# Performance work log

Measured on AMD Instinct MI355X. Metric: run time of the kernel, lower is better.

The kernel has to match this reference:

```python
import jax, jax.numpy as jnp
import numpy as np

B, S, D_MODEL = 1, 4096, 1024
D_QK = 1024
H = 32
HEAD_D = D_QK // H      # 32
V_D = D_MODEL // H      # 32
K_CONV = 4
C_CONV = D_MODEL + 2 * D_QK  # 3072 (conv_type='full')


def setup_inputs() -> dict:
    key = jax.random.key(0)
    ks = jax.random.split(key, 7)
    s_in = 1.0 / np.sqrt(D_MODEL)
    return {
        "x": jax.random.normal(ks[0], (B, S, D_MODEL), jnp.float32),
        "Wqkv_w": jax.random.normal(ks[1], (2 * D_QK + D_MODEL, D_MODEL), jnp.float32) * s_in,
        "Wqkv_b": jax.random.normal(ks[2], (2 * D_QK + D_MODEL,), jnp.float32) * 0.01,
        "conv_w": jax.random.normal(ks[3], (C_CONV, 1, K_CONV), jnp.float32) * (1.0 / np.sqrt(K_CONV)),
        "conv_b": jax.random.normal(ks[4], (C_CONV,), jnp.float32) * 0.01,
        "out_w": jax.random.normal(ks[5], (D_MODEL, D_MODEL), jnp.float32) * s_in,
        "out_b": jax.random.normal(ks[6], (D_MODEL,), jnp.float32) * 0.01,
    }


def reference(x, Wqkv_w, Wqkv_b, conv_w, conv_b, out_w, out_b):
    # QKV projection: (B,S,3072)
    qkv = x @ Wqkv_w.T + Wqkv_b
    # depthwise causal conv over seq dim (torch pads k-1 both sides, truncates to S == left-pad k-1)
    z = qkv.transpose(0, 2, 1)  # (B,C,S)
    z = jax.lax.conv_general_dilated(
        z, conv_w, window_strides=(1,), padding=[(K_CONV - 1, 0)],
        dimension_numbers=("NCH", "OIH", "NCH"), feature_group_count=C_CONV)
    z = z + conv_b[None, :, None]
    qkv = jax.nn.silu(z).transpose(0, 2, 1)  # (B,S,C)

    qk = qkv[..., : 2 * D_QK].reshape(B, S, 2, H, HEAD_D)
    v = qkv[..., 2 * D_QK :].reshape(B, S, H, V_D)
    q, k = qk[:, :, 0], qk[:, :, 1]
    q = jax.nn.elu(q) + 1.0
    k = jax.nn.elu(k) + 1.0

    # linear attention via cumulative KV state: (B,S,H,D,Dv)
    kv = jnp.einsum("bshd,bsht->bshdt", k, v)
    kv = jnp.cumsum(kv, axis=1)
    k_cum = jnp.cumsum(k, axis=1)
    denom = jnp.einsum("bshd,bshd->bsh", q, k_cum)
    ctx = jnp.einsum("bshd,bshdt->bsht", q, kv) / denom[..., None]  # (B,S,H,Dv)

    out = ctx.reshape(B, S, D_MODEL) @ out_w.T + out_b
    return out
```

## Files before the change

### kernel.cpp

```cpp
#include <hip/hip_runtime.h>
#include <hip/hip_bf16.h>
#include <math.h>

#define S_LEN 4096
#define D_MODEL 1024
#define C_CONV 3072
#define H_HEADS 32
#define HEAD_D 32
#define V_D 32
#define K_CONV 4
#define CHUNK 64
#define NCH (S_LEN / CHUNK)
#define SC_STRIDE (HEAD_D * V_D + HEAD_D)

typedef __attribute__((ext_vector_type(8))) short short8;
typedef __attribute__((ext_vector_type(4))) float f32x4;

#define F4C(v, k) ((k) == 0 ? (v).x : (k) == 1 ? (v).y : (k) == 2 ? (v).z : (v).w)

__device__ __forceinline__ ushort f32_to_bf16_rne(float f) {
  unsigned u = __float_as_uint(f);
  unsigned rounding = 0x7FFFu + ((u >> 16) & 1u);
  return (ushort)((u + rounding) >> 16);
}

__device__ __forceinline__ void gload_lds16(const void* g, void* l) {
  __builtin_amdgcn_global_load_lds(
      (const __attribute__((address_space(1))) void*)g,
      (__attribute__((address_space(3))) void*)l, 16, 0, 0);
}

__global__ __launch_bounds__(256) void split_bf16(
    const float* __restrict__ in, ushort* __restrict__ hi,
    ushort* __restrict__ lo, int n4) {
  int i = blockIdx.x * 256 + threadIdx.x;
  const int stride = gridDim.x * 256;
  for (; i < n4; i += stride) {
    const float4 v = reinterpret_cast<const float4*>(in)[i];
    float arr[4] = {v.x, v.y, v.z, v.w};
    ushort hh[4], ll[4];
#pragma unroll
    for (int j = 0; j < 4; ++j) {
      const ushort hb = f32_to_bf16_rne(arr[j]);
      const float hf = __uint_as_float((unsigned)hb << 16);
      hh[j] = hb;
      ll[j] = f32_to_bf16_rne(arr[j] - hf);
    }
    ushort4 h = {hh[0], hh[1], hh[2], hh[3]};
    ushort4 lw = {ll[0], ll[1], ll[2], ll[3]};
    reinterpret_cast<ushort4*>(hi)[i] = h;
    reinterpret_cast<ushort4*>(lo)[i] = lw;
  }
}

#define GBM 128
#define GBK 32

template <int NF>
__global__ __launch_bounds__(256, 4) void gemm_nt_split3(
    const ushort* __restrict__ Ah, const ushort* __restrict__ Al,
    const ushort* __restrict__ Bh, const ushort* __restrict__ Bl,
    const float* __restrict__ bias, float* __restrict__ C,
    int M, int N, int K) {
  constexpr int BN = NF * 32;
  __shared__ ushort lds[8192 + 2 * BN * 32];
  ushort* sAh = lds;
  ushort* sAl = lds + 4096;
  ushort* sBh = lds + 8192;
  ushort* sBl = lds + 8192 + BN * 32;

  const int t = threadIdx.x;
  const int l = t & 63;
  const int w = t >> 6;
  const int wr = w >> 1;
  const int wc = w & 1;
  const int bm = blockIdx.y * GBM;
  const int bn = blockIdx.x * BN;
  const int r16 = l & 15;
  const int g = l >> 4;

  f32x4 acc[4][NF];
#pragma unroll
  for (int m = 0; m < 4; ++m)
#pragma unroll
    for (int n = 0; n < NF; ++n) acc[m][n] = {0.f, 0.f, 0.f, 0.f};

  auto stage = [&](const ushort* __restrict__ G, ushort* Lt, int base_row,
                   int k0, int nu ) {
    for (int u0 = 0; u0 < nu; u0 += 256) {
      const int u = u0 + t;
      const int row = u >> 2;
      const int sp = u & 3;
      const int sg = sp ^ ((row >> 1) & 3);
      gload_lds16(&G[(size_t)(base_row + row) * K + k0 + sg * 8], &Lt[u * 8]);
    }
  };

  for (int k0 = 0; k0 < K; k0 += GBK) {
    stage(Ah, sAh, bm, k0, 512);
    stage(Al, sAl, bm, k0, 512);
    stage(Bh, sBh, bn, k0, BN * 4);
    stage(Bl, sBl, bn, k0, BN * 4);
    __syncthreads();

    short8 afh[4], afl[4], bfh[NF], bfl[NF];
#pragma unroll
    for (int m = 0; m < 4; ++m) {
      const int arow = wr * 64 + m * 16 + r16;
      const int off = arow * 64 + (((g ^ ((arow >> 1) & 3))) << 4);
      afh[m] = *reinterpret_cast<const short8*>((const char*)sAh + off);
      afl[m] = *reinterpret_cast<const short8*>((const char*)sAl + off);
    }
#pragma unroll
    for (int n = 0; n < NF; ++n) {
      const int brow = wc * (NF * 16) + n * 16 + r16;
      const int off = brow * 64 + (((g ^ ((brow >> 1) & 3))) << 4);
      bfh[n] = *reinterpret_cast<const short8*>((const char*)sBh + off);
      bfl[n] = *reinterpret_cast<const short8*>((const char*)sBl + off);
    }
#pragma unroll
    for (int m = 0; m < 4; ++m)
#pragma unroll
      for (int n = 0; n < NF; ++n) {
        acc[m][n] = __builtin_amdgcn_mfma_f32_16x16x32_bf16(
            afh[m], bfh[n], acc[m][n], 0, 0, 0);
        acc[m][n] = __builtin_amdgcn_mfma_f32_16x16x32_bf16(
            afh[m], bfl[n], acc[m][n], 0, 0, 0);
        acc[m][n] = __builtin_amdgcn_mfma_f32_16x16x32_bf16(
            afl[m], bfh[n], acc[m][n], 0, 0, 0);
      }
    __syncthreads();
  }

#pragma unroll
  for (int n = 0; n < NF; ++n) {
    const int col = bn + wc * (NF * 16) + n * 16 + r16;
    const float bb = bias[col];
#pragma unroll
    for (int m = 0; m < 4; ++m) {
      const int row0 = bm + wr * 64 + m * 16 + g * 4;
#pragma unroll
      for (int j = 0; j < 4; ++j)
        C[(size_t)(row0 + j) * N + col] = acc[m][n][j] + bb;
    }
  }
}

__global__ __launch_bounds__(256) void conv_silu_act(
    const float* __restrict__ qkv, const float* __restrict__ conv_w,
    const float* __restrict__ conv_b, float* __restrict__ act) {
  const int gid = blockIdx.x * 256 + threadIdx.x;
  const int nc4 = C_CONV / 4;
  if (gid >= S_LEN * nc4) return;
  const int s = gid / nc4;
  const int c = (gid % nc4) * 4;

  float w[4][4];
#pragma unroll
  for (int cc = 0; cc < 4; ++cc) {
    const float4 wv = *reinterpret_cast<const float4*>(&conv_w[(c + cc) * 4]);
    w[cc][0] = wv.x; w[cc][1] = wv.y; w[cc][2] = wv.z; w[cc][3] = wv.w;
  }
  const float4 bv = *reinterpret_cast<const float4*>(&conv_b[c]);
  float z[4] = {bv.x, bv.y, bv.z, bv.w};

#pragma unroll
  for (int j = 0; j < 4; ++j) {
    const int sp = s - 3 + j;
    if (sp >= 0) {
      const float4 in = *reinterpret_cast<const float4*>(
          &qkv[(size_t)sp * C_CONV + c]);
      z[0] += in.x * w[0][j]; z[1] += in.y * w[1][j];
      z[2] += in.z * w[2][j]; z[3] += in.w * w[3][j];
    }
  }

  float out[4];
  const bool is_qk = (c < 2 * D_MODEL);
#pragma unroll
  for (int cc = 0; cc < 4; ++cc) {
    float a = z[cc] / (1.0f + expf(-z[cc]));
    if (is_qk) a = (a > 0.0f) ? (a + 1.0f) : expf(a);
    out[cc] = a;
  }
  float4 ov = {out[0], out[1], out[2], out[3]};
  *reinterpret_cast<float4*>(&act[(size_t)s * C_CONV + c]) = ov;
}

__global__ __launch_bounds__(256) void chunk_sums(
    const float* __restrict__ act, float* __restrict__ SC) {
  const int ch = blockIdx.x;
  const int h = blockIdx.y;
  const int t = threadIdx.x;
  __shared__ float ks[CHUNK][32];
  __shared__ float vs[CHUNK][36];

#pragma unroll
  for (int i = 0; i < 2; ++i) {
    int idx = t + 256 * i;
    int r = idx >> 3;
    int c0 = (idx & 7) * 4;
    const size_t row = (size_t)(ch * CHUNK + r) * C_CONV;
    const float4 kv4 = *reinterpret_cast<const float4*>(
        &act[row + D_MODEL + h * 32 + c0]);
    *reinterpret_cast<float4*>(&ks[r][c0]) = kv4;
    const float4 vv4 = *reinterpret_cast<const float4*>(
        &act[row + 2 * D_MODEL + h * 32 + c0]);
    *reinterpret_cast<float4*>(&vs[r][c0]) = vv4;
  }
  __syncthreads();

  const int d = t >> 3;
  const int c4 = (t & 7) * 4;
  float4 acc = {0.f, 0.f, 0.f, 0.f};
  float ksum = 0.f;
#pragma unroll 4
  for (int s = 0; s < CHUNK; ++s) {
    const float kv = ks[s][d];
    const float4 vv = *reinterpret_cast<const float4*>(&vs[s][c4]);
    acc.x += kv * vv.x; acc.y += kv * vv.y;
    acc.z += kv * vv.z; acc.w += kv * vv.w;
    ksum += kv;
  }
  float* out = &SC[(size_t)(ch * H_HEADS + h) * SC_STRIDE];
  *reinterpret_cast<float4*>(&out[d * 32 + c4]) = acc;
  if ((t & 7) == 0) out[1024 + d] = ksum;
}

__global__ __launch_bounds__(256) void chunk_prefix(
    const float* __restrict__ SC, float* __restrict__ SP) {
  const int h = blockIdx.x;
  const int t = threadIdx.x;
  for (int e = t; e < SC_STRIDE; e += 256) {
    float run = 0.f;
    for (int c = 0; c < NCH; ++c) {
      const size_t off = (size_t)(c * H_HEADS + h) * SC_STRIDE + e;
      SP[off] = run;
      run += SC[off];
    }
  }
}

__global__ __launch_bounds__(256) void chunk_ctx(
    const float* __restrict__ act, const float* __restrict__ SP,
    ushort* __restrict__ ctx_h, ushort* __restrict__ ctx_l) {
  const int ch = blockIdx.x;
  const int h = blockIdx.y;
  const int t = threadIdx.x;

  __shared__ float qs[CHUNK][36];
  __shared__ float ksT[32][68];
  __shared__ float vs[CHUNK][36];
  __shared__ float KVp[32][36];
  __shared__ float Amat[CHUNK][68];
  __shared__ float Kp[32];
  __shared__ float denomp[CHUNK][4];
  __shared__ float denom[CHUNK];

#pragma unroll
  for (int i = 0; i < 2; ++i) {
    const int idx = t + 256 * i;
    const int r = idx >> 3;
    const int c0 = (idx & 7) * 4;
    const size_t row = (size_t)(ch * CHUNK + r) * C_CONV;
    float4 v4;
    v4 = *reinterpret_cast<const float4*>(&act[row + h * 32 + c0]);
    *reinterpret_cast<float4*>(&qs[r][c0]) = v4;
    v4 = *reinterpret_cast<const float4*>(&act[row + D_MODEL + h * 32 + c0]);
    ksT[c0 + 0][r] = v4.x; ksT[c0 + 1][r] = v4.y;
    ksT[c0 + 2][r] = v4.z; ksT[c0 + 3][r] = v4.w;
    v4 = *reinterpret_cast<const float4*>(&act[row + 2 * D_MODEL + h * 32 + c0]);
    *reinterpret_cast<float4*>(&vs[r][c0]) = v4;
  }
  const float* sp = &SP[(size_t)(ch * H_HEADS + h) * SC_STRIDE];
  {
    const float4 v4 = *reinterpret_cast<const float4*>(&sp[t * 4]);
    *reinterpret_cast<float4*>(&KVp[t >> 3][(t & 7) * 4]) = v4;
  }
  if (t < 32) Kp[t] = sp[1024 + t];
  __syncthreads();

  {
    const int tm = t >> 4;
    const int tn = t & 15;
    float a1[4][4] = {{0.f}};
#pragma unroll
    for (int g = 0; g < 8; ++g) {
      const int d0 = g * 4;
      float4 qv[4], kq[4];
#pragma unroll
      for (int i = 0; i < 4; ++i)
        qv[i] = *reinterpret_cast<const float4*>(&qs[tm * 4 + i][d0]);
#pragma unroll
      for (int dd = 0; dd < 4; ++dd)
        kq[dd] = *reinterpret_cast<const float4*>(&ksT[d0 + dd][tn * 4]);
#pragma unroll
      for (int i = 0; i < 4; ++i)
#pragma unroll
        for (int dd = 0; dd < 4; ++dd) {
          const float qa = F4C(qv[i], dd);
          a1[i][0] += qa * kq[dd].x;
          a1[i][1] += qa * kq[dd].y;
          a1[i][2] += qa * kq[dd].z;
          a1[i][3] += qa * kq[dd].w;
        }
    }
#pragma unroll
    for (int i = 0; i < 4; ++i) {
      const int s = tm * 4 + i;
      float4 o;
      o.x = (tn * 4 + 0 <= s) ? a1[i][0] : 0.f;
      o.y = (tn * 4 + 1 <= s) ? a1[i][1] : 0.f;
      o.z = (tn * 4 + 2 <= s) ? a1[i][2] : 0.f;
      o.w = (tn * 4 + 3 <= s) ? a1[i][3] : 0.f;
      *reinterpret_cast<float4*>(&Amat[s][tn * 4]) = o;
    }
  }
  __syncthreads();

  {
    const int row = t & 63;
    const int qd = t >> 6;
    float part = 0.f;
#pragma unroll
    for (int j = 0; j < 16; ++j) part += Amat[row][qd * 16 + j];
    if (qd < 2) {
#pragma unroll
      for (int j = 0; j < 16; ++j)
        part += qs[row][qd * 16 + j] * Kp[qd * 16 + j];
    }
    denomp[row][qd] = part;
  }
  __syncthreads();
  if (t < CHUNK) {
    const float4 dp = *reinterpret_cast<const float4*>(&denomp[t][0]);
    denom[t] = dp.x + dp.y + dp.z + dp.w;
  }
  __syncthreads();

  {
    const int r2 = t >> 3;
    const int c4 = (t & 7) * 4;
    float a3[2][4] = {{0.f}};
#pragma unroll
    for (int sg = 0; sg < 16; ++sg) {
      const int s0 = sg * 4;
      float4 av[2];
      av[0] = *reinterpret_cast<const float4*>(&Amat[r2 * 2 + 0][s0]);
      av[1] = *reinterpret_cast<const float4*>(&Amat[r2 * 2 + 1][s0]);
      float4 vv[4];
#pragma unroll
      for (int ss = 0; ss < 4; ++ss)
        vv[ss] = *reinterpret_cast<const float4*>(&vs[s0 + ss][c4]);
#pragma unroll
      for (int i = 0; i < 2; ++i)
#pragma unroll
        for (int ss = 0; ss < 4; ++ss) {
          const float aa = F4C(av[i], ss);
          a3[i][0] += aa * vv[ss].x;
          a3[i][1] += aa * vv[ss].y;
          a3[i][2] += aa * vv[ss].z;
          a3[i][3] += aa * vv[ss].w;
        }
    }
#pragma unroll
    for (int g = 0; g < 8; ++g) {
      const int d0 = g * 4;
      float4 qv[2];
      qv[0] = *reinterpret_cast<const float4*>(&qs[r2 * 2 + 0][d0]);
      qv[1] = *reinterpret_cast<const float4*>(&qs[r2 * 2 + 1][d0]);
      float4 kv[4];
#pragma unroll
      for (int dd = 0; dd < 4; ++dd)
        kv[dd] = *reinterpret_cast<const float4*>(&KVp[d0 + dd][c4]);
#pragma unroll
      for (int i = 0; i < 2; ++i)
#pragma unroll
        for (int dd = 0; dd < 4; ++dd) {
          const float qa = F4C(qv[i], dd);
          a3[i][0] += qa * kv[dd].x;
          a3[i][1] += qa * kv[dd].y;
          a3[i][2] += qa * kv[dd].z;
          a3[i][3] += qa * kv[dd].w;
        }
    }
#pragma unroll
    for (int i = 0; i < 2; ++i) {
      const int srow = r2 * 2 + i;
      const float dn = denom[srow];
      const size_t off = (size_t)(ch * CHUNK + srow) * D_MODEL + h * 32 + c4;
      ushort4 hv, lv;
      ushort hh[4], ll[4];
#pragma unroll
      for (int c = 0; c < 4; ++c) {
        const float val = a3[i][c] / dn;
        const ushort hb = f32_to_bf16_rne(val);
        hh[c] = hb;
        ll[c] = f32_to_bf16_rne(val - __uint_as_float((unsigned)hb << 16));
      }
      hv.x = hh[0]; hv.y = hh[1]; hv.z = hh[2]; hv.w = hh[3];
      lv.x = ll[0]; lv.y = ll[1]; lv.z = ll[2]; lv.w = ll[3];
      *reinterpret_cast<ushort4*>(&ctx_h[off]) = hv;
      *reinterpret_cast<ushort4*>(&ctx_l[off]) = lv;
    }
  }
}

extern "C" void kernel_launch(void* const* d_in, const int* in_sizes, int n_in,
                              void* d_out, int out_size, void* d_ws, size_t ws_size,
                              hipStream_t stream) {
  const float* x      = (const float*)d_in[0];
  const float* Wqkv_w = (const float*)d_in[1];
  const float* Wqkv_b = (const float*)d_in[2];
  const float* conv_w = (const float*)d_in[3];
  const float* conv_b = (const float*)d_in[4];
  const float* out_w  = (const float*)d_in[5];
  const float* out_b  = (const float*)d_in[6];
  float* out = (float*)d_out;

  char* ws = (char*)d_ws;
  float*  qkv_raw = (float*)(ws);
  float*  SC      = (float*)(ws);
  float*  SP      = (float*)(ws + 8650752);
  ushort* ch      = (ushort*)(ws + 17301504);
  ushort* cl      = (ushort*)(ws + 25690112);
  float*  act     = (float*)(ws + 50331648);
  ushort* xh      = (ushort*)(ws + 50331648);
  ushort* xl      = (ushort*)(ws + 58720256);
  ushort* wh      = (ushort*)(ws + 67108864);
  ushort* wl      = (ushort*)(ws + 73400320);
  ushort* oh      = (ushort*)(ws + 50331648);
  ushort* ol      = (ushort*)(ws + 52428800);

  split_bf16<<<2048, 256, 0, stream>>>(x, xh, xl, S_LEN * D_MODEL / 4);
  split_bf16<<<2048, 256, 0, stream>>>(Wqkv_w, wh, wl, C_CONV * D_MODEL / 4);

  {
    dim3 grid(C_CONV / 128, S_LEN / GBM);
    gemm_nt_split3<4><<<grid, 256, 0, stream>>>(xh, xl, wh, wl, Wqkv_b,
                                                qkv_raw, S_LEN, C_CONV,
                                                D_MODEL);
  }
  {
    int total = S_LEN * (C_CONV / 4);
    conv_silu_act<<<(total + 255) / 256, 256, 0, stream>>>(qkv_raw, conv_w,
                                                           conv_b, act);
  }
  {
    dim3 grid(NCH, H_HEADS);
    chunk_sums<<<grid, 256, 0, stream>>>(act, SC);
  }
  chunk_prefix<<<H_HEADS, 256, 0, stream>>>(SC, SP);
  {
    dim3 grid(NCH, H_HEADS);
    chunk_ctx<<<grid, 256, 0, stream>>>(act, SP, ch, cl);
  }
  split_bf16<<<1024, 256, 0, stream>>>(out_w, oh, ol, D_MODEL * D_MODEL / 4);
  {
    dim3 grid(D_MODEL / 64, S_LEN / GBM);
    gemm_nt_split3<2><<<grid, 256, 0, stream>>>(ch, cl, oh, ol, out_b, out,
                                                S_LEN, D_MODEL, D_MODEL);
  }
}
```

Before: 325.9 us.

## Merge input splits, parallelize chunk prefix, widen output GEMM tile

Fuses the two bf16 hi/lo split launches for x and Wqkv into one kernel, saving a launch. Spreads chunk_prefix over a 2D grid so each thread handles one state element instead of looping over several per head, which raises parallelism in that serial scan. Also switches the output projection GEMM from a 64-wide to a 128-wide N tile. The wider tile halves the block count to 256, which may under-fill the GPU's compute units.

```diff
diff --git a/kernel.cpp b/kernel.cpp
--- a/kernel.cpp
+++ b/kernel.cpp
@@ -30,26 +30,43 @@
       (__attribute__((address_space(3))) void*)l, 16, 0, 0);
 }
 
+__device__ __forceinline__ void split_one4(const float* __restrict__ in,
+                                           ushort* __restrict__ hi,
+                                           ushort* __restrict__ lo, int i) {
+  const float4 v = reinterpret_cast<const float4*>(in)[i];
+  float arr[4] = {v.x, v.y, v.z, v.w};
+  ushort hh[4], ll[4];
+#pragma unroll
+  for (int j = 0; j < 4; ++j) {
+    const ushort hb = f32_to_bf16_rne(arr[j]);
+    const float hf = __uint_as_float((unsigned)hb << 16);
+    hh[j] = hb;
+    ll[j] = f32_to_bf16_rne(arr[j] - hf);
+  }
+  ushort4 h = {hh[0], hh[1], hh[2], hh[3]};
+  ushort4 lw = {ll[0], ll[1], ll[2], ll[3]};
+  reinterpret_cast<ushort4*>(hi)[i] = h;
+  reinterpret_cast<ushort4*>(lo)[i] = lw;
+}
+
 __global__ __launch_bounds__(256) void split_bf16(
     const float* __restrict__ in, ushort* __restrict__ hi,
     ushort* __restrict__ lo, int n4) {
   int i = blockIdx.x * 256 + threadIdx.x;
   const int stride = gridDim.x * 256;
-  for (; i < n4; i += stride) {
-    const float4 v = reinterpret_cast<const float4*>(in)[i];
-    float arr[4] = {v.x, v.y, v.z, v.w};
-    ushort hh[4], ll[4];
-#pragma unroll
-    for (int j = 0; j < 4; ++j) {
-      const ushort hb = f32_to_bf16_rne(arr[j]);
-      const float hf = __uint_as_float((unsigned)hb << 16);
-      hh[j] = hb;
-      ll[j] = f32_to_bf16_rne(arr[j] - hf);
-    }
-    ushort4 h = {hh[0], hh[1], hh[2], hh[3]};
-    ushort4 lw = {ll[0], ll[1], ll[2], ll[3]};
-    reinterpret_cast<ushort4*>(hi)[i] = h;
-    reinterpret_cast<ushort4*>(lo)[i] = lw;
+  for (; i < n4; i += stride) split_one4(in, hi, lo, i);
+}
+
+__global__ __launch_bounds__(256) void split_bf16_x2(
+    const float* __restrict__ a, ushort* __restrict__ ah,
+    ushort* __restrict__ al, int n4a,
+    const float* __restrict__ b, ushort* __restrict__ bh,
+    ushort* __restrict__ bl, int n4b) {
+  const int gid = blockIdx.x * 256 + threadIdx.x;
+  if (gid < n4a) {
+    split_one4(a, ah, al, gid);
+  } else if (gid < n4a + n4b) {
+    split_one4(b, bh, bl, gid - n4a);
   }
 }
 
@@ -229,15 +246,14 @@
 
 __global__ __launch_bounds__(256) void chunk_prefix(
     const float* __restrict__ SC, float* __restrict__ SP) {
-  const int h = blockIdx.x;
-  const int t = threadIdx.x;
-  for (int e = t; e < SC_STRIDE; e += 256) {
-    float run = 0.f;
-    for (int c = 0; c < NCH; ++c) {
-      const size_t off = (size_t)(c * H_HEADS + h) * SC_STRIDE + e;
-      SP[off] = run;
-      run += SC[off];
-    }
+  const int h = blockIdx.y;
+  const int e = blockIdx.x * 256 + threadIdx.x;
+  if (e >= SC_STRIDE) return;
+  float run = 0.f;
+  for (int c = 0; c < NCH; ++c) {
+    const size_t off = (size_t)(c * H_HEADS + h) * SC_STRIDE + e;
+    SP[off] = run;
+    run += SC[off];
   }
 }
 
@@ -432,8 +448,9 @@
   ushort* oh      = (ushort*)(ws + 50331648);
   ushort* ol      = (ushort*)(ws + 52428800);
 
-  split_bf16<<<2048, 256, 0, stream>>>(x, xh, xl, S_LEN * D_MODEL / 4);
-  split_bf16<<<2048, 256, 0, stream>>>(Wqkv_w, wh, wl, C_CONV * D_MODEL / 4);
+  split_bf16_x2<<<7168, 256, 0, stream>>>(
+      x, xh, xl, S_LEN * D_MODEL / 4,
+      Wqkv_w, wh, wl, C_CONV * D_MODEL / 4);
 
   {
     dim3 grid(C_CONV / 128, S_LEN / GBM);
@@ -450,15 +467,18 @@
     dim3 grid(NCH, H_HEADS);
     chunk_sums<<<grid, 256, 0, stream>>>(act, SC);
   }
-  chunk_prefix<<<H_HEADS, 256, 0, stream>>>(SC, SP);
+  {
+    dim3 grid((SC_STRIDE + 255) / 256, H_HEADS);
+    chunk_prefix<<<grid, 256, 0, stream>>>(SC, SP);
+  }
   {
     dim3 grid(NCH, H_HEADS);
     chunk_ctx<<<grid, 256, 0, stream>>>(act, SP, ch, cl);
   }
   split_bf16<<<1024, 256, 0, stream>>>(out_w, oh, ol, D_MODEL * D_MODEL / 4);
   {
-    dim3 grid(D_MODEL / 64, S_LEN / GBM);
-    gemm_nt_split3<2><<<grid, 256, 0, stream>>>(ch, cl, oh, ol, out_b, out,
+    dim3 grid(D_MODEL / 128, S_LEN / GBM);
+    gemm_nt_split3<4><<<grid, 256, 0, stream>>>(ch, cl, oh, ol, out_b, out,
                                                 S_LEN, D_MODEL, D_MODEL);
   }
 }
```

New measurement: 321.3 us. Within noise of the previous version (-1.4%).
